# Kernel optimization log

Measured on AMD Instinct MI355X. Metric: run time of the kernel, lower is better.

Reference implementation:

```python
import jax, jax.numpy as jnp
import numpy as np

N, SEQ_LEN, HORIZON, F_IN, EMBED, HIDDEN, LAYERS = 4096, 168, 24, 32, 32, 64, 2
G4 = 4 * HIDDEN
# NOTE: original torch code calls nn.LSTM per-step WITHOUT carrying hidden state,
# so each step's LSTM starts from (h0=0, c0=0): W_hh contributes nothing, only b_hh.

def setup_inputs() -> dict:
    key = jax.random.key(0)
    ks = jax.random.split(key, 12)
    s = 0.1
    return {
        "X": jax.random.normal(ks[0], (N, SEQ_LEN, F_IN), jnp.float32),
        "y": jax.random.normal(ks[1], (N, SEQ_LEN), jnp.float32),
        "Xf": jax.random.normal(ks[2], (N, HORIZON, F_IN), jnp.float32),
        "W_embed": jax.random.normal(ks[3], (EMBED, 1), jnp.float32) * s,
        "b_embed": jax.random.normal(ks[4], (EMBED,), jnp.float32) * s,
        "W_ih": jax.random.normal(ks[5], (LAYERS, G4, EMBED + F_IN), jnp.float32) * s,  # layer1 in-dim == HIDDEN == EMBED+F_IN
        "b_ih": jax.random.normal(ks[6], (LAYERS, G4), jnp.float32) * s,
        "b_hh": jax.random.normal(ks[7], (LAYERS, G4), jnp.float32) * s,
        "W_mu": jax.random.normal(ks[8], (1, HIDDEN), jnp.float32) * s,
        "b_mu": jax.random.normal(ks[9], (1,), jnp.float32) * s,
        "W_sigma": jax.random.normal(ks[10], (1, HIDDEN), jnp.float32) * s,
        "b_sigma": jax.random.normal(ks[11], (1,), jnp.float32) * s,
    }


def reference(X, y, Xf, W_embed, b_embed, W_ih, b_ih, b_hh, W_mu, b_mu, W_sigma, b_sigma):
    num_ts = X.shape[0]
    T = SEQ_LEN + HORIZON
    Xall = jnp.concatenate([X, Xf], axis=1)  # (N, T, F_IN)
    y_pad = jnp.concatenate([y, jnp.zeros((num_ts, HORIZON), y.dtype)], axis=1)  # (N, T)
    use_y = jnp.arange(T) < SEQ_LEN  # teacher-forced region

    def step(carry, inputs):
        x_s, y_s, use = inputs  # (N, F_IN), (N,), scalar bool
        ynext = jnp.where(use, y_s[:, None], carry)  # (N, 1)
        yembed = ynext @ W_embed.T + b_embed  # (N, EMBED)
        h = jnp.concatenate([x_s, yembed], axis=1)  # (N, F_IN+EMBED)
        for l in range(LAYERS):  # single LSTM step from zero state per layer
            gates = h @ W_ih[l].T + b_ih[l] + b_hh[l]  # (N, 4H); torch gate order i,f,g,o
            i_g, f_g, g_g, o_g = jnp.split(gates, 4, axis=1)
            c = jax.nn.sigmoid(i_g) * jnp.tanh(g_g)  # f * c0 term vanishes (c0 = 0)
            h = jax.nn.sigmoid(o_g) * jnp.tanh(c)
        h = jax.nn.relu(h)
        mu = h @ W_mu.T + b_mu  # (N, 1)
        sigma = jax.nn.softplus(h @ W_sigma.T + b_sigma) + 1e-6  # log(1+exp(.)) + eps
        lik = (2.0 * np.pi * sigma ** 2) ** (-0.5) * jnp.exp(-((ynext - mu) ** 2) / (2.0 * sigma ** 2))
        return lik, (lik[:, 0], mu[:, 0], sigma[:, 0])

    carry0 = jnp.zeros((num_ts, 1), X.dtype)
    xs = (jnp.swapaxes(Xall, 0, 1), y_pad.T, use_y)
    _, (lik_t, mu_t, sigma_t) = jax.lax.scan(step, carry0, xs)  # each (T, N)
    ypred = lik_t.T[:, SEQ_LEN - 1: SEQ_LEN + HORIZON - 1]  # (N, HORIZON)
    return ypred, mu_t.T, sigma_t.T
```

## Files before the change

kernel.cpp:

```cpp
#include <hip/hip_runtime.h>
#include <math.h>

#define N_TS 4096
#define SEQ  168
#define HOR  24
#define T_ALL 192
#define F_INP 32
#define HID  64
#define NROW 192
#define HPAD 72
#define L2E  1.44269504089f

typedef _Float16 half8  __attribute__((ext_vector_type(8)));
typedef _Float16 half4  __attribute__((ext_vector_type(4)));
typedef float    floatx4 __attribute__((ext_vector_type(4)));

__device__ __forceinline__ float fexp(float x)  { return __expf(x); }
__device__ __forceinline__ float ex2(float x)   { return __builtin_amdgcn_exp2f(x); }
__device__ __forceinline__ float frcp(float x)  { return __builtin_amdgcn_rcpf(x); }
__device__ __forceinline__ float softplus_(float x) { return (x > 15.0f) ? x : __logf(1.0f + fexp(x)); }

__device__ __forceinline__ float lstm_h(float ip, float gp, float op) {
    const float Ei = ex2(ip);
    const float Eg = ex2(gp);
    const float cc = (1.0f - Eg) * frcp((1.0f + Ei) * (1.0f + Eg));
    const float Ec = ex2(cc * (-2.0f * L2E));
    const float Eo = ex2(op);
    return (1.0f - Ec) * frcp((1.0f + Ec) * (1.0f + Eo));
}

__device__ __forceinline__ half8 cvt8(const float4 a, const float4 b) {
    half8 v;
    v[0]=(_Float16)a.x; v[1]=(_Float16)a.y; v[2]=(_Float16)a.z; v[3]=(_Float16)a.w;
    v[4]=(_Float16)b.x; v[5]=(_Float16)b.y; v[6]=(_Float16)b.z; v[7]=(_Float16)b.w;
    return v;
}

__global__ __launch_bounds__(256) void prep(
    const float* __restrict__ W_ih, const float* __restrict__ b_ih,
    const float* __restrict__ b_hh,
    _Float16* __restrict__ W16f, float* __restrict__ bsum)
{
    const int idx = blockIdx.x * 256 + threadIdx.x;
    for (int i = idx; i < 2 * 8 * NROW * 8; i += gridDim.x * 256) {
        const int kp  = i & 7;
        const int row = (i >> 3) % NROW;
        const int kb  = ((i >> 3) / NROW) & 7;
        const int l   = i / (8 * NROW * 8);
        const int sr  = (row < 64) ? row : row + 64;
        const float sc = (row >= 64 && row < 128) ? (-2.0f * L2E) : (-L2E);
        W16f[i] = (_Float16)(W_ih[(l * 256 + sr) * HID + kb * 8 + kp] * sc);
    }
    for (int i = idx; i < 2 * NROW; i += gridDim.x * 256) {
        const int r = i % NROW;
        const int l = i / NROW;
        const int sr = (r < 64) ? r : r + 64;
        const float sc = (r >= 64 && r < 128) ? (-2.0f * L2E) : (-L2E);
        bsum[i] = (b_ih[l * 256 + sr] + b_hh[l * 256 + sr]) * sc;
    }
}

__global__ __launch_bounds__(256, 4) void cellsA(
    const float* __restrict__ X,
    const float* __restrict__ y,
    const float* __restrict__ W_embed,
    const float* __restrict__ b_embed,
    const _Float16* __restrict__ W16f,
    const float* __restrict__ bsum,
    const float* __restrict__ W_mu,
    const float* __restrict__ b_mu,
    const float* __restrict__ W_sigma,
    const float* __restrict__ b_sigma,
    float* __restrict__ out,
    float* __restrict__ lik167)
{
    __shared__ __align__(16) _Float16 Wl[NROW * HID];
    __shared__ __align__(16) _Float16 Hx[4][16 * HPAD];
    const int tid  = threadIdx.x;
    const int w    = tid >> 6;
    const int lane = tid & 63;
    const int quad = lane >> 4;
    const int ln   = lane & 15;
    const int cid0 = blockIdx.x * 64 + w * 16;
    const int cid  = cid0 + ln;

    half8 afr0, afr1;
    {
        const float* xp = X + (size_t)cid * F_INP + quad * 8;
        const float4 xa = *(const float4*)xp;
        const float4 xb = *(const float4*)(xp + 4);
        afr0 = cvt8(xa, xb);
        const float yv = y[cid];
        const float4 wa = *(const float4*)(W_embed + quad * 8);
        const float4 wb = *(const float4*)(W_embed + quad * 8 + 4);
        const float4 ba = *(const float4*)(b_embed + quad * 8);
        const float4 bb = *(const float4*)(b_embed + quad * 8 + 4);
        afr1[0]=(_Float16)fmaf(yv, wa.x, ba.x); afr1[1]=(_Float16)fmaf(yv, wa.y, ba.y);
        afr1[2]=(_Float16)fmaf(yv, wa.z, ba.z); afr1[3]=(_Float16)fmaf(yv, wa.w, ba.w);
        afr1[4]=(_Float16)fmaf(yv, wb.x, bb.x); afr1[5]=(_Float16)fmaf(yv, wb.y, bb.y);
        afr1[6]=(_Float16)fmaf(yv, wb.z, bb.z); afr1[7]=(_Float16)fmaf(yv, wb.w, bb.w);
    }

    #pragma unroll
    for (int c = 0; c < 6; ++c) {
        const int off = (c * 256 + tid) * 8;
        *(half8*)(Wl + off) = *(const half8*)(W16f + off);
    }
    __syncthreads();

    _Float16* hrow = Hx[w];
    {
        floatx4 acc[12];
        #pragma unroll
        for (int nt = 0; nt < 12; ++nt) {
            const float bv = bsum[nt * 16 + ln];
            acc[nt] = (floatx4){bv, bv, bv, bv};
        }
        const _Float16* bp = Wl + quad * 1536 + ln * 8;
        #pragma unroll
        for (int nt = 0; nt < 12; ++nt) {
            const half8 b0 = *(const half8*)(bp + nt * 128);
            const half8 b1 = *(const half8*)(bp + nt * 128 + 6144);
            acc[nt] = __builtin_amdgcn_mfma_f32_16x16x32_f16(afr0, b0, acc[nt], 0, 0, 0);
            acc[nt] = __builtin_amdgcn_mfma_f32_16x16x32_f16(afr1, b1, acc[nt], 0, 0, 0);
        }
        #pragma unroll
        for (int jt = 0; jt < 4; ++jt)
        #pragma unroll
        for (int r = 0; r < 4; ++r) {
            const float hh = lstm_h(acc[jt][r], acc[4 + jt][r], acc[8 + jt][r]);
            hrow[(quad * 4 + r) * HPAD + jt * 16 + ln] = (_Float16)hh;
        }
    }
    __syncthreads();

    #pragma unroll
    for (int c = 0; c < 6; ++c) {
        const int off = (c * 256 + tid) * 8;
        *(half8*)(Wl + off) = *(const half8*)(W16f + 12288 + off);
    }
    __syncthreads();

    float hfin[4][4];
    {
        const half8 a0 = *(const half8*)(hrow + ln * HPAD + quad * 8);
        const half8 a1 = *(const half8*)(hrow + ln * HPAD + 32 + quad * 8);
        floatx4 acc[12];
        #pragma unroll
        for (int nt = 0; nt < 12; ++nt) {
            const float bv = bsum[NROW + nt * 16 + ln];
            acc[nt] = (floatx4){bv, bv, bv, bv};
        }
        const _Float16* bp = Wl + quad * 1536 + ln * 8;
        #pragma unroll
        for (int nt = 0; nt < 12; ++nt) {
            const half8 b0 = *(const half8*)(bp + nt * 128);
            const half8 b1 = *(const half8*)(bp + nt * 128 + 6144);
            acc[nt] = __builtin_amdgcn_mfma_f32_16x16x32_f16(a0, b0, acc[nt], 0, 0, 0);
            acc[nt] = __builtin_amdgcn_mfma_f32_16x16x32_f16(a1, b1, acc[nt], 0, 0, 0);
        }
        #pragma unroll
        for (int jt = 0; jt < 4; ++jt)
        #pragma unroll
        for (int r = 0; r < 4; ++r)
            hfin[jt][r] = lstm_h(acc[jt][r], acc[4 + jt][r], acc[8 + jt][r]);
    }

    float wmu[4], wsg[4];
    #pragma unroll
    for (int jt = 0; jt < 4; ++jt) {
        wmu[jt] = W_mu[jt * 16 + ln];
        wsg[jt] = W_sigma[jt * 16 + ln];
    }
    const float bmu = b_mu[0], bsg = b_sigma[0];
    float* mu_out = out + (size_t)N_TS * HOR;
    float* sg_out = mu_out + (size_t)N_TS * T_ALL;

    #pragma unroll
    for (int r = 0; r < 4; ++r) {
        float pm = 0.f, ps = 0.f;
        #pragma unroll
        for (int jt = 0; jt < 4; ++jt) {
            const float hr = fmaxf(hfin[jt][r], 0.0f);
            pm = fmaf(hr, wmu[jt], pm);
            ps = fmaf(hr, wsg[jt], ps);
        }
        #pragma unroll
        for (int off = 1; off < 16; off <<= 1) {
            pm += __shfl_xor(pm, off, 64);
            ps += __shfl_xor(ps, off, 64);
        }
        if (ln == 0) {
            const int cid2 = cid0 + quad * 4 + r;
            const int n = cid2 / SEQ;
            const int t = cid2 - n * SEQ;
            const float mu = pm + bmu;
            const float sg = softplus_(ps + bsg) + 1e-6f;
            mu_out[(size_t)n * T_ALL + t] = mu;
            sg_out[(size_t)n * T_ALL + t] = sg;
            if (t == SEQ - 1) {
                const float yv = y[cid2];
                const float d  = yv - mu;
                const float is = frcp(sg);
                const float lik = 0.39894228040143267f * is * fexp(-0.5f * d * d * is * is);
                out[(size_t)n * HOR] = lik;
                lik167[n] = lik;
            }
        }
    }
}

__global__ __launch_bounds__(64, 1) void cellsB(
    const float* __restrict__ Xf,
    const _Float16* __restrict__ W16f,
    const float* __restrict__ bsum,
    const float* __restrict__ W_embed,
    const float* __restrict__ b_embed,
    const float* __restrict__ W_mu,
    const float* __restrict__ b_mu,
    const float* __restrict__ W_sigma,
    const float* __restrict__ b_sigma,
    float* __restrict__ out,
    const float* __restrict__ lik167)
{
    __shared__ __align__(16) _Float16 slab[16][HPAD];
    const int lane = threadIdx.x;
    const int quad = lane >> 4;
    const int ln   = lane & 15;
    const int n0   = blockIdx.x * 16;

    half8 W1f[12][2], W2f[12][2];
    #pragma unroll
    for (int nt = 0; nt < 12; ++nt)
        #pragma unroll
        for (int kf = 0; kf < 2; ++kf) {
            const int kb = kf * 4 + quad;
            W1f[nt][kf] = *(const half8*)(W16f + ((size_t)kb * NROW + nt * 16 + ln) * 8);
            W2f[nt][kf] = *(const half8*)(W16f + 12288 + ((size_t)kb * NROW + nt * 16 + ln) * 8);
        }
    float4 b1v[12], b2v[12];
    #pragma unroll
    for (int nt = 0; nt < 12; ++nt) {
        b1v[nt] = *(const float4*)(bsum + nt * 16 + quad * 4);
        b2v[nt] = *(const float4*)(bsum + NROW + nt * 16 + quad * 4);
    }
    float we[8], be[8];
    #pragma unroll
    for (int e = 0; e < 8; ++e) {
        we[e] = W_embed[quad * 8 + e];
        be[e] = b_embed[quad * 8 + e];
    }
    float4 wmuv[4], wsgv[4];
    #pragma unroll
    for (int jt = 0; jt < 4; ++jt) {
        wmuv[jt] = *(const float4*)(W_mu + jt * 16 + quad * 4);
        wsgv[jt] = *(const float4*)(W_sigma + jt * 16 + quad * 4);
    }
    const float bmu = b_mu[0], bsg = b_sigma[0];

    float yv = lik167[n0 + ln];

    float* mu_out = out + (size_t)N_TS * HOR;
    float* sg_out = mu_out + (size_t)N_TS * T_ALL;

    const float* xp = Xf + (size_t)(n0 + ln) * HOR * F_INP + quad * 8;
    float4 xa = *(const float4*)xp;
    float4 xb = *(const float4*)(xp + 4);

    #pragma unroll 1
    for (int s = 0; s < HOR; ++s) {
        const half8 xf0 = cvt8(xa, xb);
        if (s < HOR - 1) {
            xa = *(const float4*)(xp + (s + 1) * F_INP);
            xb = *(const float4*)(xp + (s + 1) * F_INP + 4);
        }
        half8 xf1;
        #pragma unroll
        for (int e = 0; e < 8; ++e)
            xf1[e] = (_Float16)fmaf(yv, we[e], be[e]);

        floatx4 acc[12];
        #pragma unroll
        for (int nt = 0; nt < 12; ++nt) {
            acc[nt] = (floatx4){b1v[nt].x, b1v[nt].y, b1v[nt].z, b1v[nt].w};
            acc[nt] = __builtin_amdgcn_mfma_f32_16x16x32_f16(W1f[nt][0], xf0, acc[nt], 0, 0, 0);
            acc[nt] = __builtin_amdgcn_mfma_f32_16x16x32_f16(W1f[nt][1], xf1, acc[nt], 0, 0, 0);
        }

        #pragma unroll
        for (int jt = 0; jt < 4; ++jt) {
            half4 hp;
            #pragma unroll
            for (int r = 0; r < 4; ++r)
                hp[r] = (_Float16)lstm_h(acc[jt][r], acc[4 + jt][r], acc[8 + jt][r]);
            *(half4*)(&slab[ln][jt * 16 + quad * 4]) = hp;
        }
        const half8 a0 = *(const half8*)(&slab[ln][quad * 8]);
        const half8 a1 = *(const half8*)(&slab[ln][32 + quad * 8]);

        #pragma unroll
        for (int nt = 0; nt < 12; ++nt) {
            acc[nt] = (floatx4){b2v[nt].x, b2v[nt].y, b2v[nt].z, b2v[nt].w};
            acc[nt] = __builtin_amdgcn_mfma_f32_16x16x32_f16(W2f[nt][0], a0, acc[nt], 0, 0, 0);
            acc[nt] = __builtin_amdgcn_mfma_f32_16x16x32_f16(W2f[nt][1], a1, acc[nt], 0, 0, 0);
        }

        float pm = 0.f, ps = 0.f;
        #pragma unroll
        for (int jt = 0; jt < 4; ++jt)
        #pragma unroll
        for (int r = 0; r < 4; ++r) {
            const float hh = lstm_h(acc[jt][r], acc[4 + jt][r], acc[8 + jt][r]);
            const float hr = fmaxf(hh, 0.0f);
            pm = fmaf(hr, ((const float*)&wmuv[jt])[r], pm);
            ps = fmaf(hr, ((const float*)&wsgv[jt])[r], ps);
        }
        pm += __shfl_xor(pm, 16, 64);  pm += __shfl_xor(pm, 32, 64);
        ps += __shfl_xor(ps, 16, 64);  ps += __shfl_xor(ps, 32, 64);

        const float mu = pm + bmu;
        const float sg = softplus_(ps + bsg) + 1e-6f;
        const float d  = yv - mu;
        const float is = frcp(sg);
        const float lik = 0.39894228040143267f * is * fexp(-0.5f * d * d * is * is);

        if (quad == 0) {
            const int nn = n0 + ln;
            const int t  = SEQ + s;
            mu_out[(size_t)nn * T_ALL + t] = mu;
            sg_out[(size_t)nn * T_ALL + t] = sg;
            if (s < HOR - 1) out[(size_t)nn * HOR + s + 1] = lik;
        }
        yv = lik;
    }
}

extern "C" void kernel_launch(void* const* d_in, const int* in_sizes, int n_in,
                              void* d_out, int out_size, void* d_ws, size_t ws_size,
                              hipStream_t stream) {
    const float* X       = (const float*)d_in[0];
    const float* y       = (const float*)d_in[1];
    const float* Xf      = (const float*)d_in[2];
    const float* W_embed = (const float*)d_in[3];
    const float* b_embed = (const float*)d_in[4];
    const float* W_ih    = (const float*)d_in[5];
    const float* b_ih    = (const float*)d_in[6];
    const float* b_hh    = (const float*)d_in[7];
    const float* W_mu    = (const float*)d_in[8];
    const float* b_mu    = (const float*)d_in[9];
    const float* W_sigma = (const float*)d_in[10];
    const float* b_sigma = (const float*)d_in[11];

    float* out = (float*)d_out;
    float*     lik167 = (float*)d_ws;
    _Float16*  W16f   = (_Float16*)((char*)d_ws + 16384);
    float*     bsum   = (float*)((char*)d_ws + 16384 + 49152);

    prep<<<96, 256, 0, stream>>>(W_ih, b_ih, b_hh, W16f, bsum);

    cellsA<<<(N_TS * SEQ) / 64, 256, 0, stream>>>(
        X, y, W_embed, b_embed, W16f, bsum,
        W_mu, b_mu, W_sigma, b_sigma, out, lik167);

    cellsB<<<N_TS / 16, 64, 0, stream>>>(
        Xf, W16f, bsum, W_embed, b_embed,
        W_mu, b_mu, W_sigma, b_sigma, out, lik167);
}
```

Before: 284.4 us.

## Cut register pressure in LSTM cells; stage layer-2 weights in LDS for cellsB

```diff
diff --git a/kernel.cpp b/kernel.cpp
--- a/kernel.cpp
+++ b/kernel.cpp
@@ -8,7 +8,6 @@
 #define F_INP 32
 #define HID  64
 #define NROW 192
-#define HPAD 72
 #define L2E  1.44269504089f
 
 typedef _Float16 half8  __attribute__((ext_vector_type(8)));
@@ -60,7 +59,7 @@
     }
 }
 
-__global__ __launch_bounds__(256, 4) void cellsA(
+__global__ __launch_bounds__(256, 5) void cellsA(
     const float* __restrict__ X,
     const float* __restrict__ y,
     const float* __restrict__ W_embed,
@@ -75,7 +74,7 @@
     float* __restrict__ lik167)
 {
     __shared__ __align__(16) _Float16 Wl[NROW * HID];
-    __shared__ __align__(16) _Float16 Hx[4][16 * HPAD];
+    __shared__ __align__(16) _Float16 Hx[4][16 * 64];
     const int tid  = threadIdx.x;
     const int w    = tid >> 6;
     const int lane = tid & 63;
@@ -110,30 +109,35 @@
 
     _Float16* hrow = Hx[w];
     {
-        floatx4 acc[12];
-        #pragma unroll
-        for (int nt = 0; nt < 12; ++nt) {
-            const float bv = bsum[nt * 16 + ln];
-            acc[nt] = (floatx4){bv, bv, bv, bv};
-        }
         const _Float16* bp = Wl + quad * 1536 + ln * 8;
         #pragma unroll
-        for (int nt = 0; nt < 12; ++nt) {
-            const half8 b0 = *(const half8*)(bp + nt * 128);
-            const half8 b1 = *(const half8*)(bp + nt * 128 + 6144);
-            acc[nt] = __builtin_amdgcn_mfma_f32_16x16x32_f16(afr0, b0, acc[nt], 0, 0, 0);
-            acc[nt] = __builtin_amdgcn_mfma_f32_16x16x32_f16(afr1, b1, acc[nt], 0, 0, 0);
-        }
-        #pragma unroll
-        for (int jt = 0; jt < 4; ++jt)
-        #pragma unroll
-        for (int r = 0; r < 4; ++r) {
-            const float hh = lstm_h(acc[jt][r], acc[4 + jt][r], acc[8 + jt][r]);
-            hrow[(quad * 4 + r) * HPAD + jt * 16 + ln] = (_Float16)hh;
-        }
-    }
+        for (int jt = 0; jt < 4; ++jt) {
+            const float bi = bsum[jt * 16 + ln];
+            const float bg = bsum[(4 + jt) * 16 + ln];
+            const float bo = bsum[(8 + jt) * 16 + ln];
+            floatx4 ai = (floatx4){bi, bi, bi, bi};
+            floatx4 ag = (floatx4){bg, bg, bg, bg};
+            floatx4 ao = (floatx4){bo, bo, bo, bo};
+            ai = __builtin_amdgcn_mfma_f32_16x16x32_f16(afr0, *(const half8*)(bp + jt * 128),            ai, 0, 0, 0);
+            ai = __builtin_amdgcn_mfma_f32_16x16x32_f16(afr1, *(const half8*)(bp + jt * 128 + 6144),     ai, 0, 0, 0);
+            ag = __builtin_amdgcn_mfma_f32_16x16x32_f16(afr0, *(const half8*)(bp + (4 + jt) * 128),      ag, 0, 0, 0);
+            ag = __builtin_amdgcn_mfma_f32_16x16x32_f16(afr1, *(const half8*)(bp + (4 + jt) * 128 + 6144), ag, 0, 0, 0);
+            ao = __builtin_amdgcn_mfma_f32_16x16x32_f16(afr0, *(const half8*)(bp + (8 + jt) * 128),      ao, 0, 0, 0);
+            ao = __builtin_amdgcn_mfma_f32_16x16x32_f16(afr1, *(const half8*)(bp + (8 + jt) * 128 + 6144), ao, 0, 0, 0);
+            #pragma unroll
+            for (int r = 0; r < 4; ++r) {
+                const float hh = lstm_h(ai[r], ag[r], ao[r]);
+                const int row = quad * 4 + r;
+                const int col = jt * 16 + ln;
+                hrow[row * 64 + (((col >> 3) ^ (row & 7)) << 3) + (col & 7)] = (_Float16)hh;
+            }
+        }
+    }
+
+    const half8 a0 = *(const half8*)(hrow + ln * 64 + ((quad ^ (ln & 7)) << 3));
+    const half8 a1 = *(const half8*)(hrow + ln * 64 + (((4 + quad) ^ (ln & 7)) << 3));
+
     __syncthreads();
-
     #pragma unroll
     for (int c = 0; c < 6; ++c) {
         const int off = (c * 256 + tid) * 8;
@@ -143,27 +147,25 @@
 
     float hfin[4][4];
     {
-        const half8 a0 = *(const half8*)(hrow + ln * HPAD + quad * 8);
-        const half8 a1 = *(const half8*)(hrow + ln * HPAD + 32 + quad * 8);
-        floatx4 acc[12];
-        #pragma unroll
-        for (int nt = 0; nt < 12; ++nt) {
-            const float bv = bsum[NROW + nt * 16 + ln];
-            acc[nt] = (floatx4){bv, bv, bv, bv};
-        }
         const _Float16* bp = Wl + quad * 1536 + ln * 8;
         #pragma unroll
-        for (int nt = 0; nt < 12; ++nt) {
-            const half8 b0 = *(const half8*)(bp + nt * 128);
-            const half8 b1 = *(const half8*)(bp + nt * 128 + 6144);
-            acc[nt] = __builtin_amdgcn_mfma_f32_16x16x32_f16(a0, b0, acc[nt], 0, 0, 0);
-            acc[nt] = __builtin_amdgcn_mfma_f32_16x16x32_f16(a1, b1, acc[nt], 0, 0, 0);
-        }
-        #pragma unroll
-        for (int jt = 0; jt < 4; ++jt)
-        #pragma unroll
-        for (int r = 0; r < 4; ++r)
-            hfin[jt][r] = lstm_h(acc[jt][r], acc[4 + jt][r], acc[8 + jt][r]);
+        for (int jt = 0; jt < 4; ++jt) {
+            const float bi = bsum[NROW + jt * 16 + ln];
+            const float bg = bsum[NROW + (4 + jt) * 16 + ln];
+            const float bo = bsum[NROW + (8 + jt) * 16 + ln];
+            floatx4 ai = (floatx4){bi, bi, bi, bi};
+            floatx4 ag = (floatx4){bg, bg, bg, bg};
+            floatx4 ao = (floatx4){bo, bo, bo, bo};
+            ai = __builtin_amdgcn_mfma_f32_16x16x32_f16(a0, *(const half8*)(bp + jt * 128),            ai, 0, 0, 0);
+            ai = __builtin_amdgcn_mfma_f32_16x16x32_f16(a1, *(const half8*)(bp + jt * 128 + 6144),     ai, 0, 0, 0);
+            ag = __builtin_amdgcn_mfma_f32_16x16x32_f16(a0, *(const half8*)(bp + (4 + jt) * 128),      ag, 0, 0, 0);
+            ag = __builtin_amdgcn_mfma_f32_16x16x32_f16(a1, *(const half8*)(bp + (4 + jt) * 128 + 6144), ag, 0, 0, 0);
+            ao = __builtin_amdgcn_mfma_f32_16x16x32_f16(a0, *(const half8*)(bp + (8 + jt) * 128),      ao, 0, 0, 0);
+            ao = __builtin_amdgcn_mfma_f32_16x16x32_f16(a1, *(const half8*)(bp + (8 + jt) * 128 + 6144), ao, 0, 0, 0);
+            #pragma unroll
+            for (int r = 0; r < 4; ++r)
+                hfin[jt][r] = lstm_h(ai[r], ag[r], ao[r]);
+        }
     }
 
     float wmu[4], wsg[4];
@@ -223,27 +225,34 @@
     float* __restrict__ out,
     const float* __restrict__ lik167)
 {
-    __shared__ __align__(16) _Float16 slab[16][HPAD];
+    __shared__ __align__(16) _Float16 W2l[12288];
+    __shared__ __align__(16) float    b2l[NROW];
+    __shared__ __align__(16) _Float16 slab[16 * 72];
     const int lane = threadIdx.x;
     const int quad = lane >> 4;
     const int ln   = lane & 15;
     const int n0   = blockIdx.x * 16;
 
-    half8 W1f[12][2], W2f[12][2];
+    #pragma unroll
+    for (int c = 0; c < 24; ++c) {
+        const int off = (c * 64 + lane) * 8;
+        *(half8*)(W2l + off) = *(const half8*)(W16f + 12288 + off);
+    }
+    #pragma unroll
+    for (int c = 0; c < 3; ++c)
+        b2l[c * 64 + lane] = bsum[NROW + c * 64 + lane];
+    __builtin_amdgcn_s_waitcnt(0);
+
+    half8 W1f[12][2];
     #pragma unroll
     for (int nt = 0; nt < 12; ++nt)
         #pragma unroll
-        for (int kf = 0; kf < 2; ++kf) {
-            const int kb = kf * 4 + quad;
-            W1f[nt][kf] = *(const half8*)(W16f + ((size_t)kb * NROW + nt * 16 + ln) * 8);
-            W2f[nt][kf] = *(const half8*)(W16f + 12288 + ((size_t)kb * NROW + nt * 16 + ln) * 8);
-        }
-    float4 b1v[12], b2v[12];
-    #pragma unroll
-    for (int nt = 0; nt < 12; ++nt) {
+        for (int kf = 0; kf < 2; ++kf)
+            W1f[nt][kf] = *(const half8*)(W16f + ((size_t)(kf * 4 + quad) * NROW + nt * 16 + ln) * 8);
+    float4 b1v[12];
+    #pragma unroll
+    for (int nt = 0; nt < 12; ++nt)
         b1v[nt] = *(const float4*)(bsum + nt * 16 + quad * 4);
-        b2v[nt] = *(const float4*)(bsum + NROW + nt * 16 + quad * 4);
-    }
     float we[8], be[8];
     #pragma unroll
     for (int e = 0; e < 8; ++e) {
@@ -293,16 +302,20 @@
             #pragma unroll
             for (int r = 0; r < 4; ++r)
                 hp[r] = (_Float16)lstm_h(acc[jt][r], acc[4 + jt][r], acc[8 + jt][r]);
-            *(half4*)(&slab[ln][jt * 16 + quad * 4]) = hp;
-        }
-        const half8 a0 = *(const half8*)(&slab[ln][quad * 8]);
-        const half8 a1 = *(const half8*)(&slab[ln][32 + quad * 8]);
+            *(half4*)(&slab[ln * 72 + jt * 16 + quad * 4]) = hp;
+        }
+        const half8 a0 = *(const half8*)(&slab[ln * 72 + quad * 8]);
+        const half8 a1 = *(const half8*)(&slab[ln * 72 + 32 + quad * 8]);
 
         #pragma unroll
         for (int nt = 0; nt < 12; ++nt) {
-            acc[nt] = (floatx4){b2v[nt].x, b2v[nt].y, b2v[nt].z, b2v[nt].w};
-            acc[nt] = __builtin_amdgcn_mfma_f32_16x16x32_f16(W2f[nt][0], a0, acc[nt], 0, 0, 0);
-            acc[nt] = __builtin_amdgcn_mfma_f32_16x16x32_f16(W2f[nt][1], a1, acc[nt], 0, 0, 0);
+            const floatx4 bi = *(const floatx4*)(b2l + nt * 16 + quad * 4);
+            floatx4 a = bi;
+            a = __builtin_amdgcn_mfma_f32_16x16x32_f16(
+                    *(const half8*)(W2l + ((size_t)quad * NROW + nt * 16 + ln) * 8), a0, a, 0, 0, 0);
+            a = __builtin_amdgcn_mfma_f32_16x16x32_f16(
+                    *(const half8*)(W2l + ((size_t)(4 + quad) * NROW + nt * 16 + ln) * 8), a1, a, 0, 0, 0);
+            acc[nt] = a;
         }
 
         float pm = 0.f, ps = 0.f;
```

Result: no change. 282.4 us (-0.7%).
